# Kernel tuning notes

Measured on AMD Instinct MI355X. Metric: run time of the kernel, lower is better.

The kernel has to match this reference:

```python
import jax, jax.numpy as jnp
import numpy as np

NUM_HEADS = 16
ROPE_THETA = 10000.0


def apply_rope(x):
    # x: (B, H, T, hd), interleaved-pair RoPE (rotary-embedding-torch convention)
    T, hd = x.shape[-2], x.shape[-1]
    inv_freq = 1.0 / (ROPE_THETA ** (jnp.arange(0, hd, 2, dtype=jnp.float32) / hd))  # (hd/2,)
    ang = jnp.arange(T, dtype=jnp.float32)[:, None] * inv_freq[None, :]  # (T, hd/2)
    cos, sin = jnp.cos(ang), jnp.sin(ang)
    x1 = x[..., 0::2]
    x2 = x[..., 1::2]
    r1 = x1 * cos - x2 * sin
    r2 = x1 * sin + x2 * cos
    return jnp.stack([r1, r2], axis=-1).reshape(x.shape)


def setup_inputs() -> dict:
    key = jax.random.key(0)
    ks = jax.random.split(key, 8)
    L, S, B, E = 2048, 2048, 2, 1024
    sc = 1.0 / np.sqrt(E)
    return {
        "query": jax.random.normal(ks[0], (L, B, E), jnp.float32),
        "key": jax.random.normal(ks[1], (S, B, E), jnp.float32),
        "value": jax.random.normal(ks[2], (S, B, E), jnp.float32),
        "key_padding_mask": jnp.zeros((B, S), dtype=bool),
        "Wq": jax.random.normal(ks[3], (E, E), jnp.float32) * sc,
        "bq": jnp.zeros((E,), jnp.float32),
        "Wk": jax.random.normal(ks[4], (E, E), jnp.float32) * sc,
        "bk": jnp.zeros((E,), jnp.float32),
        "Wv": jax.random.normal(ks[5], (E, E), jnp.float32) * sc,
        "bv": jnp.zeros((E,), jnp.float32),
        "Wo": jax.random.normal(ks[6], (E, E), jnp.float32) * sc,
        "bo": jnp.zeros((E,), jnp.float32),
    }


def reference(query, key, value, key_padding_mask, Wq, bq, Wk, bk, Wv, bv, Wo, bo):
    L, B, E = query.shape
    S = key.shape[0]
    H = NUM_HEADS
    hd = E // H
    # projections (torch Linear: x @ W.T + b)
    Q = query @ Wq.T + bq  # (L, B, E)
    K = key @ Wk.T + bk    # (S, B, E)
    V = value @ Wv.T + bv  # (S, B, E)
    # (T, B, E) -> (B, H, T, hd)
    Q = Q.reshape(L, B, H, hd).transpose(1, 2, 0, 3)
    K = K.reshape(S, B, H, hd).transpose(1, 2, 0, 3)
    V = V.reshape(S, B, H, hd).transpose(1, 2, 0, 3)
    Q = apply_rope(Q)
    K = apply_rope(K)
    scores = jnp.einsum("bhld,bhsd->bhls", Q, K) / jnp.sqrt(jnp.float32(hd))
    scores = jnp.where(key_padding_mask[:, None, None, :], -jnp.inf, scores)
    attn = jax.nn.softmax(scores, axis=-1)
    out = jnp.einsum("bhls,bhsd->bhld", attn, V)  # (B, H, L, hd)
    out = out.transpose(2, 0, 1, 3).reshape(L, B, E)
    return out @ Wo.T + bo
```

## Files before the change

### kernel.cpp

```cpp
#include <hip/hip_runtime.h>
#include <hip/hip_bf16.h>

typedef __hip_bfloat16 bf16;
typedef short bf16x8 __attribute__((ext_vector_type(8)));
typedef float f32x4 __attribute__((ext_vector_type(4)));
typedef short s4 __attribute__((ext_vector_type(4)));

#define LL 2048
#define SS 2048
#define EE 1024
#define HH 16
#define HD 64
#define MM (LL * 2)

static __device__ __forceinline__ short f2bs(float f) {
  bf16 h = __float2bfloat16(f);
  short u;
  __builtin_memcpy(&u, &h, 2);
  return u;
}

static __device__ __forceinline__ void st8(bf16* p, float4 x, float4 y) {
  bf16x8 v;
  v[0] = f2bs(x.x); v[1] = f2bs(x.y); v[2] = f2bs(x.z); v[3] = f2bs(x.w);
  v[4] = f2bs(y.x); v[5] = f2bs(y.y); v[6] = f2bs(y.z); v[7] = f2bs(y.w);
  *(bf16x8*)p = v;
}

#define GLL16(gp, lp) __builtin_amdgcn_global_load_lds(                        \
    (const __attribute__((address_space(1))) void*)(gp),                       \
    (__attribute__((address_space(3))) void*)(lp), 16, 0, 0)

__global__ __launch_bounds__(256) void prep_kernel(
    float2* __restrict__ tab, const unsigned char* __restrict__ m,
    float* __restrict__ mf,
    const float* __restrict__ s0, const float* __restrict__ s1,
    const float* __restrict__ s2, const float* __restrict__ s3,
    bf16* __restrict__ wdst) {
  const int bid = blockIdx.x;
  if (bid < 256) {
    int i = bid * 256 + threadIdx.x;
    int pos = i >> 5, fi = i & 31;
    float freq = expf(-(float)fi * (9.210340371976184f / 32.0f));
    float ang = (float)pos * freq;
    float s, c;
    sincosf(ang, &s, &c);
    tab[i] = make_float2(c, s);
  } else if (bid < 272) {
    int i = (bid - 256) * 256 + threadIdx.x;
    if (i < 2 * SS) mf[i] = m[i] ? -1e30f : 0.f;
  } else {
    int b2 = bid - 272;
    int sel = b2 >> 10;
    const float* src = (sel == 0) ? s0 : (sel == 1) ? s1 : (sel == 2) ? s2 : s3;
    size_t loc = ((size_t)(b2 & 1023) * 256 + threadIdx.x) * 4;
    float4 v = *(const float4*)(src + loc);
    s4 p;
    p[0] = f2bs(v.x); p[1] = f2bs(v.y); p[2] = f2bs(v.z); p[3] = f2bs(v.w);
    *(s4*)(wdst + (size_t)sel * EE * EE + loc) = p;
  }
}

template<int MODE, bool XB16, bool WB16>
__global__ __launch_bounds__(256) void proj_kernel(
    const void* __restrict__ Xv, const void* __restrict__ Wv,
    const float* __restrict__ bias, void* __restrict__ dstv,
    const float2* __restrict__ tab)
{
  const int w = threadIdx.x >> 6;
  const int lane = threadIdx.x & 63;
  const int l15 = lane & 15, quad = lane >> 4;
  const int tm = blockIdx.x * 128 + w * 32;
  const int tn = blockIdx.y * 64;

  const size_t aoff0 = (size_t)(tm + l15) * EE + quad * 8;
  const size_t aoff1 = aoff0 + (size_t)16 * EE;
  const size_t woff  = (size_t)(tn + l15) * EE + quad * 8;

  f32x4 zero4 = {0.f, 0.f, 0.f, 0.f};
  f32x4 acc[2][4];
#pragma unroll
  for (int mi = 0; mi < 2; ++mi)
#pragma unroll
    for (int ni = 0; ni < 4; ++ni) acc[mi][ni] = zero4;

  for (int k0 = 0; k0 < EE; k0 += 32) {
    bf16x8 a0, a1;
    if (XB16 || MODE == 3) {
      const bf16* Xb = (const bf16*)Xv;
      a0 = *(const bf16x8*)(Xb + aoff0 + k0);
      a1 = *(const bf16x8*)(Xb + aoff1 + k0);
    } else {
      const float* Xf = (const float*)Xv;
#pragma unroll
      for (int j = 0; j < 8; ++j) a0[j] = f2bs(Xf[aoff0 + k0 + j]);
#pragma unroll
      for (int j = 0; j < 8; ++j) a1[j] = f2bs(Xf[aoff1 + k0 + j]);
    }
#pragma unroll
    for (int ni = 0; ni < 4; ++ni) {
      bf16x8 bv;
      if (WB16) {
        const bf16* Wb = (const bf16*)Wv;
        bv = *(const bf16x8*)(Wb + woff + (size_t)ni * 16 * EE + k0);
      } else {
        const float* Wf = (const float*)Wv;
#pragma unroll
        for (int j = 0; j < 8; ++j) bv[j] = f2bs(Wf[woff + (size_t)ni * 16 * EE + k0 + j]);
      }
      acc[0][ni] = __builtin_amdgcn_mfma_f32_16x16x32_bf16(a0, bv, acc[0][ni], 0, 0, 0);
      acc[1][ni] = __builtin_amdgcn_mfma_f32_16x16x32_bf16(a1, bv, acc[1][ni], 0, 0, 0);
    }
  }

  float bz[4];
#pragma unroll
  for (int ni = 0; ni < 4; ++ni) bz[ni] = bias[tn + ni * 16 + l15];

#pragma unroll
  for (int mi = 0; mi < 2; ++mi) {
#pragma unroll
    for (int ni = 0; ni < 4; ++ni) {
      const int n = tn + ni * 16 + l15;
#pragma unroll
      for (int r = 0; r < 4; ++r) {
        const int m = tm + mi * 16 + quad * 4 + r;
        float v = acc[mi][ni][r] + bz[ni];
        if (MODE <= 1) {
          float other = __shfl_xor(v, 1, 64);
          int pos = m >> 1, b = m & 1, d = n & 63, h = n >> 6;
          float2 cs = tab[pos * 32 + (d >> 1)];
          float rv = (d & 1) ? (other * cs.y + v * cs.x) : (v * cs.x - other * cs.y);
          ((bf16*)dstv)[((size_t)(b * HH + h) * LL + pos) * HD + d] = __float2bfloat16(rv);
        } else if (MODE == 2) {
          int pos = m >> 1, b = m & 1, d = n & 63, h = n >> 6;
          ((bf16*)dstv)[((size_t)(b * HH + h) * HD + d) * SS + pos] = __float2bfloat16(v);
        } else {
          ((float*)dstv)[(size_t)m * EE + n] = v;
        }
      }
    }
  }
}

__global__ __launch_bounds__(256, 6) void qkv_kernel(
    const float* __restrict__ Xq, const float* __restrict__ Xk,
    const float* __restrict__ Xv, const bf16* __restrict__ Wb,
    const float* __restrict__ bq, const float* __restrict__ bk,
    const float* __restrict__ bv, bf16* __restrict__ Qr,
    bf16* __restrict__ Kr, bf16* __restrict__ Vt,
    const float2* __restrict__ tab)
{
  __shared__ __align__(16) bf16 As[2][4096];
  __shared__ __align__(16) bf16 Bs[2][2048];

  const int tid = threadIdx.x;
  const int w = tid >> 6;
  const int lane = tid & 63;
  const int l15 = lane & 15, quad = lane >> 4;
  const int id = blockIdx.x;
  const int z = id >> 9;
  const int g = id & 511;
  const int tmb = (g & 31) * 128;
  const int tn  = (g >> 5) * 64;

  const float* Xf = (z == 0) ? Xq : (z == 1) ? Xk : Xv;
  const bf16* Wm  = Wb + (size_t)z * EE * EE;
  const float* bias = (z == 0) ? bq : (z == 1) ? bk : bv;
  bf16* dst = (z == 0) ? Qr : (z == 1) ? Kr : Vt;

  const int ar = tid >> 2;
  const int akc = tid & 3;
  const float* gA0 = Xf + (size_t)(tmb + ar) * EE + akc * 8;
  const float* gA1 = gA0 + (size_t)64 * EE;
  const int aw0 = (ar >> 1) * 64 + (((((ar & 1) << 2) | akc) ^ ((ar >> 1) & 7)) * 8);
  const int aw1 = aw0 + 2048;

  const int ub = (lane & 7) ^ (lane >> 3);
  const bf16* gB = Wm + (size_t)(tn + w * 16 + 2 * (lane >> 3) + (ub >> 2)) * EE
                      + (ub & 3) * 8;

  const int arbase = (l15 >> 1) * 64 + (((((l15 & 1) << 2) | quad) ^ (l15 >> 1)) * 8);

  f32x4 zero4 = {0.f, 0.f, 0.f, 0.f};
  f32x4 acc[2][4];
#pragma unroll
  for (int mi = 0; mi < 2; ++mi)
#pragma unroll
    for (int ni = 0; ni < 4; ++ni) acc[mi][ni] = zero4;

  {
    float4 a00 = *(const float4*)(gA0);
    float4 a01 = *(const float4*)(gA0 + 4);
    float4 a10 = *(const float4*)(gA1);
    float4 a11 = *(const float4*)(gA1 + 4);
    GLL16(gB, (bf16*)&Bs[0][w * 512] + lane * 8);
    st8(&As[0][aw0], a00, a01);
    st8(&As[0][aw1], a10, a11);
  }
  __syncthreads();

  for (int t = 0; t < 32; ++t) {
    const int cur = t & 1;
    float4 a00, a01, a10, a11;
    if (t < 31) {
      const int k0 = (t + 1) * 32;
      a00 = *(const float4*)(gA0 + k0);
      a01 = *(const float4*)(gA0 + k0 + 4);
      a10 = *(const float4*)(gA1 + k0);
      a11 = *(const float4*)(gA1 + k0 + 4);
      GLL16(gB + k0, (bf16*)&Bs[cur ^ 1][w * 512] + lane * 8);
    }
    bf16x8 af0 = *(const bf16x8*)(&As[cur][w * 1024 + arbase]);
    bf16x8 af1 = *(const bf16x8*)(&As[cur][w * 1024 + 512 + arbase]);
#pragma unroll
    for (int ni = 0; ni < 4; ++ni) {
      bf16x8 bfr = *(const bf16x8*)(&Bs[cur][ni * 512 + arbase]);
      acc[0][ni] = __builtin_amdgcn_mfma_f32_16x16x32_bf16(af0, bfr, acc[0][ni], 0, 0, 0);
      acc[1][ni] = __builtin_amdgcn_mfma_f32_16x16x32_bf16(af1, bfr, acc[1][ni], 0, 0, 0);
    }
    if (t < 31) {
      st8(&As[cur ^ 1][aw0], a00, a01);
      st8(&As[cur ^ 1][aw1], a10, a11);
    }
    __syncthreads();
  }

  float bz[4];
#pragma unroll
  for (int ni = 0; ni < 4; ++ni) bz[ni] = bias[tn + ni * 16 + l15];

#pragma unroll
  for (int mi = 0; mi < 2; ++mi) {
#pragma unroll
    for (int ni = 0; ni < 4; ++ni) {
      const int n = tn + ni * 16 + l15;
#pragma unroll
      for (int r = 0; r < 4; ++r) {
        const int m = tmb + w * 32 + mi * 16 + quad * 4 + r;
        float v = acc[mi][ni][r] + bz[ni];
        if (z <= 1) {
          float other = __shfl_xor(v, 1, 64);
          int pos = m >> 1, b = m & 1, d = n & 63, h = n >> 6;
          float2 cs = tab[pos * 32 + (d >> 1)];
          float rv = (d & 1) ? (other * cs.y + v * cs.x) : (v * cs.x - other * cs.y);
          dst[((size_t)(b * HH + h) * LL + pos) * HD + d] = __float2bfloat16(rv);
        } else {
          int pos = m >> 1, b = m & 1, d = n & 63, h = n >> 6;
          dst[((size_t)(b * HH + h) * HD + d) * SS + pos] = __float2bfloat16(v);
        }
      }
    }
  }
}

__global__ __launch_bounds__(256) void projo_kernel(
    const bf16* __restrict__ X, const bf16* __restrict__ W,
    const float* __restrict__ bias, float* __restrict__ dst)
{
  __shared__ __align__(16) bf16 As[2][4096];
  __shared__ __align__(16) bf16 Bs[2][2048];

  const int tid = threadIdx.x;
  const int w = tid >> 6;
  const int lane = tid & 63;
  const int l15 = lane & 15, quad = lane >> 4;
  const int tmb = blockIdx.x * 128;
  const int tn  = blockIdx.y * 64;

  const int ub = (lane & 7) ^ (lane >> 3);
  const bf16* gA0 = X + (size_t)(tmb + w * 32 + 2 * (lane >> 3) + (ub >> 2)) * EE
                       + (ub & 3) * 8;
  const bf16* gA1 = gA0 + (size_t)16 * EE;
  const bf16* gB  = W + (size_t)(tn + w * 16 + 2 * (lane >> 3) + (ub >> 2)) * EE
                       + (ub & 3) * 8;

  const int arbase = (l15 >> 1) * 64 + (((((l15 & 1) << 2) | quad) ^ (l15 >> 1)) * 8);

  f32x4 zero4 = {0.f, 0.f, 0.f, 0.f};
  f32x4 acc[2][4];
#pragma unroll
  for (int mi = 0; mi < 2; ++mi)
#pragma unroll
    for (int ni = 0; ni < 4; ++ni) acc[mi][ni] = zero4;

  GLL16(gA0, (bf16*)&As[0][w * 1024] + lane * 8);
  GLL16(gA1, (bf16*)&As[0][w * 1024 + 512] + lane * 8);
  GLL16(gB,  (bf16*)&Bs[0][w * 512] + lane * 8);
  __syncthreads();

  for (int t = 0; t < 32; ++t) {
    const int cur = t & 1;
    if (t < 31) {
      const int k0 = (t + 1) * 32;
      GLL16(gA0 + k0, (bf16*)&As[cur ^ 1][w * 1024] + lane * 8);
      GLL16(gA1 + k0, (bf16*)&As[cur ^ 1][w * 1024 + 512] + lane * 8);
      GLL16(gB + k0,  (bf16*)&Bs[cur ^ 1][w * 512] + lane * 8);
    }
    bf16x8 af0 = *(const bf16x8*)(&As[cur][w * 1024 + arbase]);
    bf16x8 af1 = *(const bf16x8*)(&As[cur][w * 1024 + 512 + arbase]);
#pragma unroll
    for (int ni = 0; ni < 4; ++ni) {
      bf16x8 bfr = *(const bf16x8*)(&Bs[cur][ni * 512 + arbase]);
      acc[0][ni] = __builtin_amdgcn_mfma_f32_16x16x32_bf16(af0, bfr, acc[0][ni], 0, 0, 0);
      acc[1][ni] = __builtin_amdgcn_mfma_f32_16x16x32_bf16(af1, bfr, acc[1][ni], 0, 0, 0);
    }
    __syncthreads();
  }

  float bz[4];
#pragma unroll
  for (int ni = 0; ni < 4; ++ni) bz[ni] = bias[tn + ni * 16 + l15];

#pragma unroll
  for (int mi = 0; mi < 2; ++mi) {
#pragma unroll
    for (int ni = 0; ni < 4; ++ni) {
      const int n = tn + ni * 16 + l15;
#pragma unroll
      for (int r = 0; r < 4; ++r) {
        const int m = tmb + w * 32 + mi * 16 + quad * 4 + r;
        dst[(size_t)m * EE + n] = acc[mi][ni][r] + bz[ni];
      }
    }
  }
}

__global__ __launch_bounds__(256, 4) void attn_kernel(
    const bf16* __restrict__ Qr, const bf16* __restrict__ Kr,
    const bf16* __restrict__ Vt, const float* __restrict__ maskf,
    bf16* __restrict__ ctx)
{
  __shared__ __align__(16) bf16 Ks[2][64 * 64];
  __shared__ __align__(16) bf16 Vs[2][64 * 64];
  __shared__ __align__(16) short Plds[4][16][56];

  const int w = threadIdx.x >> 6;
  const int lane = threadIdx.x & 63;
  const int l15 = lane & 15, quad = lane >> 4;
  const int id = blockIdx.x;
  const int bh = id & 31;
  const int qt = id >> 5;
  const int b = bh >> 4, h = bh & 15;
  const int q0 = qt * 64 + w * 16;

  const bf16* Qbh = Qr + (size_t)bh * LL * HD;
  const bf16* Kbh = Kr + (size_t)bh * SS * HD;
  const bf16* Vbh = Vt + (size_t)bh * HD * SS;
  const float* mrow = maskf + b * SS;

  bf16x8 qf0, qf1;
  {
    const bf16* qp = Qbh + (size_t)(q0 + l15) * HD + quad * 8;
    qf0 = *(const bf16x8*)(qp);
    qf1 = *(const bf16x8*)(qp + 32);
  }

  const int srow = lane >> 3;
  const int gswz = ((lane & 7) ^ srow) * 8;
  const int kswz0 = ((quad    ) ^ (l15 & 7)) * 8;
  const int kswz1 = ((quad + 4) ^ (l15 & 7)) * 8;

#define STAGE(buf, S0) {                                                       \
    _Pragma("unroll")                                                          \
    for (int i = 0; i < 2; ++i) {                                              \
      const int rb = w * 16 + i * 8;                                           \
      GLL16(Kbh + (size_t)((S0) + rb + srow) * HD + gswz,                      \
            (bf16*)&Ks[buf][rb * 64] + lane * 8);                              \
      GLL16(Vbh + (size_t)(rb + srow) * SS + (S0) + gswz,                      \
            (bf16*)&Vs[buf][rb * 64] + lane * 8);                              \
    }                                                                          \
  }

  f32x4 zero4 = {0.f, 0.f, 0.f, 0.f};
  f32x4 o[4];
#pragma unroll
  for (int t = 0; t < 4; ++t) o[t] = zero4;
  float ps = 0.f;

  STAGE(0, 0);
  __syncthreads();

  for (int t = 0; t < SS / 64; ++t) {
    const int s0 = t * 64;
    const int cur = t & 1;
    if (t + 1 < SS / 64) STAGE(cur ^ 1, s0 + 64);

#pragma unroll
    for (int ss = 0; ss < 2; ++ss) {
      const bf16* Kb = &Ks[cur][ss * 32 * 64];
      bf16x8 kf00 = *(const bf16x8*)(Kb + (l15)      * 64 + kswz0);
      bf16x8 kf01 = *(const bf16x8*)(Kb + (l15)      * 64 + kswz1);
      bf16x8 kf10 = *(const bf16x8*)(Kb + (16 + l15) * 64 + kswz0);
      bf16x8 kf11 = *(const bf16x8*)(Kb + (16 + l15) * 64 + kswz1);
      bf16x8 vf[4];
#pragma unroll
      for (int tt = 0; tt < 4; ++tt)
        vf[tt] = *(const bf16x8*)(&Vs[cur][0] + (tt * 16 + l15) * 64 +
                                  (((ss * 4 + quad) ^ (l15 & 7)) * 8));
      f32x4 mv0 = *(const f32x4*)(mrow + s0 + ss * 32 + quad * 4);
      f32x4 mv1 = *(const f32x4*)(mrow + s0 + ss * 32 + 16 + quad * 4);

      f32x4 sc0 = zero4, sc1 = zero4;
      sc0 = __builtin_amdgcn_mfma_f32_16x16x32_bf16(kf00, qf0, sc0, 0, 0, 0);
      sc0 = __builtin_amdgcn_mfma_f32_16x16x32_bf16(kf01, qf1, sc0, 0, 0, 0);
      sc1 = __builtin_amdgcn_mfma_f32_16x16x32_bf16(kf10, qf0, sc1, 0, 0, 0);
      sc1 = __builtin_amdgcn_mfma_f32_16x16x32_bf16(kf11, qf1, sc1, 0, 0, 0);
      s4 pk0, pk1;
#pragma unroll
      for (int r = 0; r < 4; ++r) {
        float p = __expf(sc0[r] * 0.125f + mv0[r]);
        ps += p; pk0[r] = f2bs(p);
      }
#pragma unroll
      for (int r = 0; r < 4; ++r) {
        float p = __expf(sc1[r] * 0.125f + mv1[r]);
        ps += p; pk1[r] = f2bs(p);
      }
      *(s4*)&Plds[w][l15][quad * 4] = pk0;
      *(s4*)&Plds[w][l15][16 + quad * 4] = pk1;
      asm volatile("" ::: "memory");
      bf16x8 pf = *(const bf16x8*)&Plds[w][l15][quad * 8];
#pragma unroll
      for (int tt = 0; tt < 4; ++tt)
        o[tt] = __builtin_amdgcn_mfma_f32_16x16x32_bf16(pf, vf[tt], o[tt], 0, 0, 0);
      asm volatile("" ::: "memory");
    }
    __syncthreads();
  }
#undef STAGE

  float lv = ps;
  lv += __shfl_xor(lv, 16, 64);
  lv += __shfl_xor(lv, 32, 64);

#pragma unroll
  for (int r = 0; r < 4; ++r) {
    float li = __shfl(lv, quad * 4 + r, 64);
    float inv = 1.0f / li;
    int q = q0 + quad * 4 + r;
#pragma unroll
    for (int t = 0; t < 4; ++t) {
      float val = o[t][r] * inv;
      ctx[(size_t)(q * 2 + b) * EE + (size_t)h * 64 + t * 16 + l15] = __float2bfloat16(val);
    }
  }
}

extern "C" void kernel_launch(void* const* d_in, const int* in_sizes, int n_in,
                              void* d_out, int out_size, void* d_ws, size_t ws_size,
                              hipStream_t stream) {
  const float* query = (const float*)d_in[0];
  const float* key   = (const float*)d_in[1];
  const float* value = (const float*)d_in[2];
  const unsigned char* mask = (const unsigned char*)d_in[3];
  const float* Wq = (const float*)d_in[4];
  const float* bq = (const float*)d_in[5];
  const float* Wk = (const float*)d_in[6];
  const float* bk = (const float*)d_in[7];
  const float* Wv = (const float*)d_in[8];
  const float* bv = (const float*)d_in[9];
  const float* Wo = (const float*)d_in[10];
  const float* bo = (const float*)d_in[11];

  char* ws = (char*)d_ws;
  const bool big = ws_size >= ((size_t)41 << 20);

  float2* tab   = (float2*)ws;
  float*  maskf = (float*)(ws + (512 << 10));
  bf16* Wb = (bf16*)(ws + ((size_t)1 << 20));
  size_t base = big ? ((size_t)9 << 20) : ((size_t)1 << 20);
  bf16* Qr  = (bf16*)(ws + base);
  bf16* Kr  = (bf16*)(ws + base + ((size_t)8 << 20));
  bf16* Vt  = (bf16*)(ws + base + ((size_t)16 << 20));
  bf16* ctx = (bf16*)(ws + base + ((size_t)24 << 20));

  prep_kernel<<<big ? 4368 : 272, 256, 0, stream>>>(
      tab, mask, maskf, Wq, Wk, Wv, Wo, Wb);

  if (big) {
    qkv_kernel<<<1536, 256, 0, stream>>>(query, key, value, Wb, bq, bk, bv,
                                         Qr, Kr, Vt, tab);
  } else {
    dim3 gp(MM / 128, EE / 64);
    proj_kernel<0, false, false><<<gp, 256, 0, stream>>>(query, Wq, bq, Qr, tab);
    proj_kernel<1, false, false><<<gp, 256, 0, stream>>>(key,   Wk, bk, Kr, tab);
    proj_kernel<2, false, false><<<gp, 256, 0, stream>>>(value, Wv, bv, Vt, tab);
  }

  attn_kernel<<<(LL / 64) * 2 * HH, 256, 0, stream>>>(Qr, Kr, Vt, maskf, ctx);

  if (big) {
    dim3 go(MM / 128, EE / 64);
    projo_kernel<<<go, 256, 0, stream>>>(ctx, Wb + (size_t)3 * EE * EE, bo, (float*)d_out);
  } else {
    dim3 gp(MM / 128, EE / 64);
    proj_kernel<3, true, false><<<gp, 256, 0, stream>>>(ctx, Wo, bo, d_out, tab);
  }
}
```

Baseline: 251.6 us.

## Pre-convert query/key inputs to bf16 and double attention rows per wave

The prep kernel now also converts query and key to bf16, staging them in the output buffer, so the QKV projection can stream the A operand for Q and K directly into LDS with global_load_lds instead of loading fp32 and converting in registers. Separately, the attention kernel now processes 32 query rows per wave (128 per block) instead of 16, reusing each staged K/V tile for two MFMA row groups and halving the grid. This trades an extra conversion pass over 16 MB of fp32 inputs and higher register pressure (launch bound occupancy hint dropped) for less redundant K/V traffic and cheaper projection loads.

```diff
diff --git a/kernel.cpp b/kernel.cpp
--- a/kernel.cpp
+++ b/kernel.cpp
@@ -36,7 +36,9 @@
     float* __restrict__ mf,
     const float* __restrict__ s0, const float* __restrict__ s1,
     const float* __restrict__ s2, const float* __restrict__ s3,
-    bf16* __restrict__ wdst) {
+    bf16* __restrict__ wdst,
+    const float* __restrict__ xq, const float* __restrict__ xk,
+    bf16* __restrict__ xqb, bf16* __restrict__ xkb) {
   const int bid = blockIdx.x;
   if (bid < 256) {
     int i = bid * 256 + threadIdx.x;
@@ -49,7 +51,7 @@
   } else if (bid < 272) {
     int i = (bid - 256) * 256 + threadIdx.x;
     if (i < 2 * SS) mf[i] = m[i] ? -1e30f : 0.f;
-  } else {
+  } else if (bid < 4368) {
     int b2 = bid - 272;
     int sel = b2 >> 10;
     const float* src = (sel == 0) ? s0 : (sel == 1) ? s1 : (sel == 2) ? s2 : s3;
@@ -58,6 +60,15 @@
     s4 p;
     p[0] = f2bs(v.x); p[1] = f2bs(v.y); p[2] = f2bs(v.z); p[3] = f2bs(v.w);
     *(s4*)(wdst + (size_t)sel * EE * EE + loc) = p;
+  } else {
+    int b2 = bid - 4368;
+    const float* src = (b2 < 4096) ? xq : xk;
+    bf16* dst = (b2 < 4096) ? xqb : xkb;
+    size_t loc = ((size_t)(b2 & 4095) * 256 + threadIdx.x) * 4;
+    float4 v = *(const float4*)(src + loc);
+    s4 p;
+    p[0] = f2bs(v.x); p[1] = f2bs(v.y); p[2] = f2bs(v.z); p[3] = f2bs(v.w);
+    *(s4*)(dst + loc) = p;
   }
 }
 
@@ -144,7 +155,7 @@
 }
 
 __global__ __launch_bounds__(256, 6) void qkv_kernel(
-    const float* __restrict__ Xq, const float* __restrict__ Xk,
+    const bf16* __restrict__ Xqb, const bf16* __restrict__ Xkb,
     const float* __restrict__ Xv, const bf16* __restrict__ Wb,
     const float* __restrict__ bq, const float* __restrict__ bk,
     const float* __restrict__ bv, bf16* __restrict__ Qr,
@@ -164,19 +175,25 @@
   const int tmb = (g & 31) * 128;
   const int tn  = (g >> 5) * 64;
 
-  const float* Xf = (z == 0) ? Xq : (z == 1) ? Xk : Xv;
+  const bool ab16 = (z <= 1);
+  const bf16* Xb  = (z == 0) ? Xqb : Xkb;
   const bf16* Wm  = Wb + (size_t)z * EE * EE;
   const float* bias = (z == 0) ? bq : (z == 1) ? bk : bv;
   bf16* dst = (z == 0) ? Qr : (z == 1) ? Kr : Vt;
 
+  const int ub = (lane & 7) ^ (lane >> 3);
+
+  const bf16* gAb0 = Xb + (size_t)(tmb + w * 32 + 2 * (lane >> 3) + (ub >> 2)) * EE
+                        + (ub & 3) * 8;
+  const bf16* gAb1 = gAb0 + (size_t)16 * EE;
+
   const int ar = tid >> 2;
   const int akc = tid & 3;
-  const float* gA0 = Xf + (size_t)(tmb + ar) * EE + akc * 8;
+  const float* gA0 = Xv + (size_t)(tmb + ar) * EE + akc * 8;
   const float* gA1 = gA0 + (size_t)64 * EE;
   const int aw0 = (ar >> 1) * 64 + (((((ar & 1) << 2) | akc) ^ ((ar >> 1) & 7)) * 8);
   const int aw1 = aw0 + 2048;
 
-  const int ub = (lane & 7) ^ (lane >> 3);
   const bf16* gB = Wm + (size_t)(tn + w * 16 + 2 * (lane >> 3) + (ub >> 2)) * EE
                       + (ub & 3) * 8;
 
@@ -190,13 +207,18 @@
     for (int ni = 0; ni < 4; ++ni) acc[mi][ni] = zero4;
 
   {
-    float4 a00 = *(const float4*)(gA0);
-    float4 a01 = *(const float4*)(gA0 + 4);
-    float4 a10 = *(const float4*)(gA1);
-    float4 a11 = *(const float4*)(gA1 + 4);
     GLL16(gB, (bf16*)&Bs[0][w * 512] + lane * 8);
-    st8(&As[0][aw0], a00, a01);
-    st8(&As[0][aw1], a10, a11);
+    if (ab16) {
+      GLL16(gAb0, (bf16*)&As[0][w * 1024] + lane * 8);
+      GLL16(gAb1, (bf16*)&As[0][w * 1024 + 512] + lane * 8);
+    } else {
+      float4 a00 = *(const float4*)(gA0);
+      float4 a01 = *(const float4*)(gA0 + 4);
+      float4 a10 = *(const float4*)(gA1);
+      float4 a11 = *(const float4*)(gA1 + 4);
+      st8(&As[0][aw0], a00, a01);
+      st8(&As[0][aw1], a10, a11);
+    }
   }
   __syncthreads();
 
@@ -205,11 +227,16 @@
     float4 a00, a01, a10, a11;
     if (t < 31) {
       const int k0 = (t + 1) * 32;
-      a00 = *(const float4*)(gA0 + k0);
-      a01 = *(const float4*)(gA0 + k0 + 4);
-      a10 = *(const float4*)(gA1 + k0);
-      a11 = *(const float4*)(gA1 + k0 + 4);
       GLL16(gB + k0, (bf16*)&Bs[cur ^ 1][w * 512] + lane * 8);
+      if (ab16) {
+        GLL16(gAb0 + k0, (bf16*)&As[cur ^ 1][w * 1024] + lane * 8);
+        GLL16(gAb1 + k0, (bf16*)&As[cur ^ 1][w * 1024 + 512] + lane * 8);
+      } else {
+        a00 = *(const float4*)(gA0 + k0);
+        a01 = *(const float4*)(gA0 + k0 + 4);
+        a10 = *(const float4*)(gA1 + k0);
+        a11 = *(const float4*)(gA1 + k0 + 4);
+      }
     }
     bf16x8 af0 = *(const bf16x8*)(&As[cur][w * 1024 + arbase]);
     bf16x8 af1 = *(const bf16x8*)(&As[cur][w * 1024 + 512 + arbase]);
@@ -219,7 +246,7 @@
       acc[0][ni] = __builtin_amdgcn_mfma_f32_16x16x32_bf16(af0, bfr, acc[0][ni], 0, 0, 0);
       acc[1][ni] = __builtin_amdgcn_mfma_f32_16x16x32_bf16(af1, bfr, acc[1][ni], 0, 0, 0);
     }
-    if (t < 31) {
+    if (!ab16 && t < 31) {
       st8(&As[cur ^ 1][aw0], a00, a01);
       st8(&As[cur ^ 1][aw1], a10, a11);
     }
@@ -326,14 +353,14 @@
   }
 }
 
-__global__ __launch_bounds__(256, 4) void attn_kernel(
+__global__ __launch_bounds__(256) void attn_kernel(
     const bf16* __restrict__ Qr, const bf16* __restrict__ Kr,
     const bf16* __restrict__ Vt, const float* __restrict__ maskf,
     bf16* __restrict__ ctx)
 {
   __shared__ __align__(16) bf16 Ks[2][64 * 64];
   __shared__ __align__(16) bf16 Vs[2][64 * 64];
-  __shared__ __align__(16) short Plds[4][16][56];
+  __shared__ __align__(16) short Plds[4][32][56];
 
   const int w = threadIdx.x >> 6;
   const int lane = threadIdx.x & 63;
@@ -342,18 +369,19 @@
   const int bh = id & 31;
   const int qt = id >> 5;
   const int b = bh >> 4, h = bh & 15;
-  const int q0 = qt * 64 + w * 16;
+  const int q0 = qt * 128 + w * 32;
 
   const bf16* Qbh = Qr + (size_t)bh * LL * HD;
   const bf16* Kbh = Kr + (size_t)bh * SS * HD;
   const bf16* Vbh = Vt + (size_t)bh * HD * SS;
   const float* mrow = maskf + b * SS;
 
-  bf16x8 qf0, qf1;
-  {
-    const bf16* qp = Qbh + (size_t)(q0 + l15) * HD + quad * 8;
-    qf0 = *(const bf16x8*)(qp);
-    qf1 = *(const bf16x8*)(qp + 32);
+  bf16x8 qf[2][2];
+#pragma unroll
+  for (int mi = 0; mi < 2; ++mi) {
+    const bf16* qp = Qbh + (size_t)(q0 + mi * 16 + l15) * HD + quad * 8;
+    qf[mi][0] = *(const bf16x8*)(qp);
+    qf[mi][1] = *(const bf16x8*)(qp + 32);
   }
 
   const int srow = lane >> 3;
@@ -373,10 +401,12 @@
   }
 
   f32x4 zero4 = {0.f, 0.f, 0.f, 0.f};
-  f32x4 o[4];
-#pragma unroll
-  for (int t = 0; t < 4; ++t) o[t] = zero4;
-  float ps = 0.f;
+  f32x4 o[2][4];
+#pragma unroll
+  for (int mi = 0; mi < 2; ++mi)
+#pragma unroll
+    for (int t = 0; t < 4; ++t) o[mi][t] = zero4;
+  float ps0 = 0.f, ps1 = 0.f;
 
   STAGE(0, 0);
   __syncthreads();
@@ -401,48 +431,59 @@
       f32x4 mv0 = *(const f32x4*)(mrow + s0 + ss * 32 + quad * 4);
       f32x4 mv1 = *(const f32x4*)(mrow + s0 + ss * 32 + 16 + quad * 4);
 
-      f32x4 sc0 = zero4, sc1 = zero4;
-      sc0 = __builtin_amdgcn_mfma_f32_16x16x32_bf16(kf00, qf0, sc0, 0, 0, 0);
-      sc0 = __builtin_amdgcn_mfma_f32_16x16x32_bf16(kf01, qf1, sc0, 0, 0, 0);
-      sc1 = __builtin_amdgcn_mfma_f32_16x16x32_bf16(kf10, qf0, sc1, 0, 0, 0);
-      sc1 = __builtin_amdgcn_mfma_f32_16x16x32_bf16(kf11, qf1, sc1, 0, 0, 0);
-      s4 pk0, pk1;
-#pragma unroll
-      for (int r = 0; r < 4; ++r) {
-        float p = __expf(sc0[r] * 0.125f + mv0[r]);
-        ps += p; pk0[r] = f2bs(p);
-      }
-#pragma unroll
-      for (int r = 0; r < 4; ++r) {
-        float p = __expf(sc1[r] * 0.125f + mv1[r]);
-        ps += p; pk1[r] = f2bs(p);
-      }
-      *(s4*)&Plds[w][l15][quad * 4] = pk0;
-      *(s4*)&Plds[w][l15][16 + quad * 4] = pk1;
+#pragma unroll
+      for (int mi = 0; mi < 2; ++mi) {
+        f32x4 sc0 = zero4, sc1 = zero4;
+        sc0 = __builtin_amdgcn_mfma_f32_16x16x32_bf16(kf00, qf[mi][0], sc0, 0, 0, 0);
+        sc0 = __builtin_amdgcn_mfma_f32_16x16x32_bf16(kf01, qf[mi][1], sc0, 0, 0, 0);
+        sc1 = __builtin_amdgcn_mfma_f32_16x16x32_bf16(kf10, qf[mi][0], sc1, 0, 0, 0);
+        sc1 = __builtin_amdgcn_mfma_f32_16x16x32_bf16(kf11, qf[mi][1], sc1, 0, 0, 0);
+        s4 pk0, pk1;
+#pragma unroll
+        for (int r = 0; r < 4; ++r) {
+          float p = __expf(sc0[r] * 0.125f + mv0[r]);
+          if (mi == 0) ps0 += p; else ps1 += p;
+          pk0[r] = f2bs(p);
+        }
+#pragma unroll
+        for (int r = 0; r < 4; ++r) {
+          float p = __expf(sc1[r] * 0.125f + mv1[r]);
+          if (mi == 0) ps0 += p; else ps1 += p;
+          pk1[r] = f2bs(p);
+        }
+        *(s4*)&Plds[w][mi * 16 + l15][quad * 4] = pk0;
+        *(s4*)&Plds[w][mi * 16 + l15][16 + quad * 4] = pk1;
+      }
       asm volatile("" ::: "memory");
-      bf16x8 pf = *(const bf16x8*)&Plds[w][l15][quad * 8];
-#pragma unroll
-      for (int tt = 0; tt < 4; ++tt)
-        o[tt] = __builtin_amdgcn_mfma_f32_16x16x32_bf16(pf, vf[tt], o[tt], 0, 0, 0);
+      bf16x8 pf0 = *(const bf16x8*)&Plds[w][l15][quad * 8];
+      bf16x8 pf1 = *(const bf16x8*)&Plds[w][16 + l15][quad * 8];
+#pragma unroll
+      for (int tt = 0; tt < 4; ++tt) {
+        o[0][tt] = __builtin_amdgcn_mfma_f32_16x16x32_bf16(pf0, vf[tt], o[0][tt], 0, 0, 0);
+        o[1][tt] = __builtin_amdgcn_mfma_f32_16x16x32_bf16(pf1, vf[tt], o[1][tt], 0, 0, 0);
+      }
       asm volatile("" ::: "memory");
     }
     __syncthreads();
   }
 #undef STAGE
 
-  float lv = ps;
-  lv += __shfl_xor(lv, 16, 64);
-  lv += __shfl_xor(lv, 32, 64);
-
-#pragma unroll
-  for (int r = 0; r < 4; ++r) {
-    float li = __shfl(lv, quad * 4 + r, 64);
-    float inv = 1.0f / li;
-    int q = q0 + quad * 4 + r;
-#pragma unroll
-    for (int t = 0; t < 4; ++t) {
-      float val = o[t][r] * inv;
-      ctx[(size_t)(q * 2 + b) * EE + (size_t)h * 64 + t * 16 + l15] = __float2bfloat16(val);
+  float lv0 = ps0; lv0 += __shfl_xor(lv0, 16, 64); lv0 += __shfl_xor(lv0, 32, 64);
+  float lv1 = ps1; lv1 += __shfl_xor(lv1, 16, 64); lv1 += __shfl_xor(lv1, 32, 64);
+
+#pragma unroll
+  for (int mi = 0; mi < 2; ++mi) {
+#pragma unroll
+    for (int r = 0; r < 4; ++r) {
+      float lv = (mi == 0) ? lv0 : lv1;
+      float li = __shfl(lv, quad * 4 + r, 64);
+      float inv = 1.0f / li;
+      int q = q0 + mi * 16 + quad * 4 + r;
+#pragma unroll
+      for (int t = 0; t < 4; ++t) {
+        float val = o[mi][t][r] * inv;
+        ctx[(size_t)(q * 2 + b) * EE + (size_t)h * 64 + t * 16 + l15] = __float2bfloat16(val);
+      }
     }
   }
 }
@@ -468,18 +509,20 @@
 
   float2* tab   = (float2*)ws;
   float*  maskf = (float*)(ws + (512 << 10));
-  bf16* Wb = (bf16*)(ws + ((size_t)1 << 20));
+  bf16* Wb  = (bf16*)(ws + ((size_t)1 << 20));
   size_t base = big ? ((size_t)9 << 20) : ((size_t)1 << 20);
   bf16* Qr  = (bf16*)(ws + base);
   bf16* Kr  = (bf16*)(ws + base + ((size_t)8 << 20));
   bf16* Vt  = (bf16*)(ws + base + ((size_t)16 << 20));
   bf16* ctx = (bf16*)(ws + base + ((size_t)24 << 20));
-
-  prep_kernel<<<big ? 4368 : 272, 256, 0, stream>>>(
-      tab, mask, maskf, Wq, Wk, Wv, Wo, Wb);
+  bf16* Xqb = (bf16*)d_out;
+  bf16* Xkb = (bf16*)d_out + (size_t)MM * EE;
+
+  prep_kernel<<<big ? 12560 : 272, 256, 0, stream>>>(
+      tab, mask, maskf, Wq, Wk, Wv, Wo, Wb, query, key, Xqb, Xkb);
 
   if (big) {
-    qkv_kernel<<<1536, 256, 0, stream>>>(query, key, value, Wb, bq, bk, bv,
+    qkv_kernel<<<1536, 256, 0, stream>>>(Xqb, Xkb, value, Wb, bq, bk, bv,
                                          Qr, Kr, Vt, tab);
   } else {
     dim3 gp(MM / 128, EE / 64);
@@ -488,7 +531,7 @@
     proj_kernel<2, false, false><<<gp, 256, 0, stream>>>(value, Wv, bv, Vt, tab);
   }
 
-  attn_kernel<<<(LL / 64) * 2 * HH, 256, 0, stream>>>(Qr, Kr, Vt, maskf, ctx);
+  attn_kernel<<<(LL / 128) * 2 * HH, 256, 0, stream>>>(Qr, Kr, Vt, maskf, ctx);
 
   if (big) {
     dim3 go(MM / 128, EE / 64);
```

Result: slower. 264.2 us (+5.0%).
